# Kernel optimization log

Measured on AMD Instinct MI355X. Metric: run time of the kernel, lower is better.

## Reference

```python
import jax, jax.numpy as jnp
import numpy as np

# GlobalWorkspaceConfig constants (from init_kwargs)
DT_MS = 1.0
NMDA_TAU_MS = 100.0
IGNITE_THR = 0.58
WTA_INH = 0.85
K_SELECT = 2


def setup_inputs() -> dict:
    key = jax.random.key(0)
    k1, _ = jax.random.split(key)
    T, N = 8192, 4096
    # binary spikes with firing prob 0.7 so the EMA crosses ignite_thr=0.58
    spikes = (jax.random.uniform(k1, (T, N)) < 0.7).astype(jnp.float32)
    nmda0 = jnp.zeros((N,), jnp.float32)  # initial nmda_state buffer
    return {"spikes": spikes, "nmda0": nmda0}


def reference(spikes, nmda0):
    T, N = spikes.shape
    alpha = DT_MS / max(NMDA_TAU_MS, 1.0)  # 0.01

    # linear EMA recurrence: nmda_t = (1-alpha)*nmda_{t-1} + alpha*s_t
    def step(nmda, s_t):
        nmda = (1.0 - alpha) * nmda + alpha * s_t
        return nmda, nmda

    nmda_final, nmda_seq = jax.lax.scan(step, nmda0, spikes)  # nmda_seq: [T, N]

    # per-step ignition test: max over neurons vs threshold
    ignited = nmda_seq.max(axis=1) >= IGNITE_THR  # [T] bool

    # per-step top-k (k-WTA). wta_inh scaling kept for faithfulness.
    k = min(K_SELECT, N)
    scores = nmda_seq * WTA_INH
    _, idx = jax.lax.top_k(scores, k)  # [T, k]

    rows = jnp.arange(T)[:, None]
    ignite_mask = jnp.zeros((T, N), jnp.float32).at[rows, idx].set(1.0)
    ignite_mask = ignite_mask * ignited[:, None].astype(jnp.float32)

    # coverage = mean of the row mask = k/N when ignited, else 0
    coverage = jnp.where(ignited, jnp.float32(k) / jnp.float32(N), jnp.float32(0.0))

    return ignite_mask, coverage, nmda_final
```

## Files before the change

kernel.cpp:

```cpp
#include <hip/hip_runtime.h>
#include <cstdint>
#include <cstddef>

#define C_DECAY 0.99f
#define C_ALPHA 0.01f
#define C_THR   0.58f
#define C_WTA   0.85f

#define NPB   16
#define TILE  256

#define EMA_STEP(x) nmda = __fadd_rn(__fmul_rn(C_DECAY, nmda), __fmul_rn(C_ALPHA, (x)))

typedef const __attribute__((address_space(1))) void g_void;
typedef __attribute__((address_space(3))) void l_void;
typedef float f32x4 __attribute__((ext_vector_type(4)));

__device__ __forceinline__ void gload_lds16(const float* g, float* l) {
  __builtin_amdgcn_global_load_lds((g_void*)g, (l_void*)l, 16, 0, 0);
}

__global__ __launch_bounds__(128)
void gw_phase1(const float* __restrict__ spikes, const float* __restrict__ nmda0,
               float* __restrict__ bnd, float* __restrict__ nmf,
               int T, int N, int Ls) {
  __shared__ float sb[2][TILE * NPB];
  const int w    = threadIdx.x >> 6;
  const int lane = threadIdx.x & 63;
  const int nblk = gridDim.x;
  const int bs   = (nblk % 8 == 0) ? ((blockIdx.x & 7) * (nblk >> 3) + (blockIdx.x >> 3))
                                   : (int)blockIdx.x;
  const int n0   = bs * NPB;
  const int ntiles = T / TILE;
  const int Lm1  = (1 << Ls) - 1;
  const int grow = lane >> 2;
  const int gc   = (lane & 3) * 4;

  if (w == 1) {
#pragma unroll
    for (int j = 0; j < TILE / 16; ++j)
      gload_lds16(spikes + (size_t)(j * 16 + grow) * N + n0 + gc, &sb[0][j * 256]);
  }
  __syncthreads();

  const int nn = lane & (NPB - 1);
  float nmda = 0.0f;
  if (w == 0) nmda = nmda0[n0 + nn];

  for (int tile = 0; tile < ntiles; ++tile) {
    const int cur = tile & 1;
    if (w == 0) {
      const float* buf = sb[cur];
      const int t0 = tile * TILE;
      float tA[16], tB[16];
#pragma unroll
      for (int i = 0; i < 16; ++i) tA[i] = buf[i * NPB + nn];
#pragma unroll
      for (int jp = 0; jp < TILE / 32; ++jp) {
#pragma unroll
        for (int i = 0; i < 16; ++i) tB[i] = buf[((2 * jp + 1) * 16 + i) * NPB + nn];
        { const int tb = t0 + 2 * jp * 16;
          if ((tb & Lm1) == 0 && lane < NPB) bnd[(size_t)(tb >> Ls) * N + n0 + lane] = nmda; }
#pragma unroll
        for (int i = 0; i < 16; ++i) EMA_STEP(tA[i]);
        if (jp < TILE / 32 - 1) {
#pragma unroll
          for (int i = 0; i < 16; ++i) tA[i] = buf[((2 * jp + 2) * 16 + i) * NPB + nn];
        }
        { const int tb = t0 + (2 * jp + 1) * 16;
          if ((tb & Lm1) == 0 && lane < NPB) bnd[(size_t)(tb >> Ls) * N + n0 + lane] = nmda; }
#pragma unroll
        for (int i = 0; i < 16; ++i) EMA_STEP(tB[i]);
      }
    } else if (tile + 1 < ntiles) {
      const int t0 = (tile + 1) * TILE;
#pragma unroll
      for (int j = 0; j < TILE / 16; ++j)
        gload_lds16(spikes + (size_t)(t0 + j * 16 + grow) * N + n0 + gc, &sb[cur ^ 1][j * 256]);
    }
    __syncthreads();
  }
  if (w == 0 && lane < NPB) nmf[n0 + lane] = nmda;
}

__device__ __forceinline__ void merge2(float& a1, int& i1, float& a2, int& i2,
                                       float b1, int j1, float b2, int j2) {
  const bool afirst = (a1 > b1) || (a1 == b1 && i1 < j1);
  const float w1 = afirst ? a1 : b1; const int wi1 = afirst ? i1 : j1;
  const float l1 = afirst ? b1 : a1; const int li1 = afirst ? j1 : i1;
  const float cc = afirst ? a2 : b2; const int ci  = afirst ? i2 : j2;
  const bool sfirst = (cc > l1) || (cc == l1 && ci < li1);
  a1 = w1; i1 = wi1;
  a2 = sfirst ? cc : l1; i2 = sfirst ? ci : li1;
}

#define LOCAL_TOP2(c, idx)                                         \
  if ((c) > a1) { a2 = a1; i2 = i1; a1 = (c); i1 = (idx); }        \
  else if ((c) > a2) { a2 = (c); i2 = (idx); }

#define EMA_ROW(sA, sB)                                                        \
  nmA.x = __fadd_rn(__fmul_rn(C_DECAY, nmA.x), __fmul_rn(C_ALPHA, (sA).x));    \
  nmA.y = __fadd_rn(__fmul_rn(C_DECAY, nmA.y), __fmul_rn(C_ALPHA, (sA).y));    \
  nmA.z = __fadd_rn(__fmul_rn(C_DECAY, nmA.z), __fmul_rn(C_ALPHA, (sA).z));    \
  nmA.w = __fadd_rn(__fmul_rn(C_DECAY, nmA.w), __fmul_rn(C_ALPHA, (sA).w));    \
  nmB.x = __fadd_rn(__fmul_rn(C_DECAY, nmB.x), __fmul_rn(C_ALPHA, (sB).x));    \
  nmB.y = __fadd_rn(__fmul_rn(C_DECAY, nmB.y), __fmul_rn(C_ALPHA, (sB).y));    \
  nmB.z = __fadd_rn(__fmul_rn(C_DECAY, nmB.z), __fmul_rn(C_ALPHA, (sB).z));    \
  nmB.w = __fadd_rn(__fmul_rn(C_DECAY, nmB.w), __fmul_rn(C_ALPHA, (sB).w));

__global__ __launch_bounds__(512)
void gw_phase2s(const float* __restrict__ spikes, const float* __restrict__ bnd,
                float* __restrict__ mask, float* __restrict__ cov,
                int T, int N, float covval) {
  const int tid  = threadIdx.x;
  const int lane = tid & 63;
  const int wv   = tid >> 6;
  const int N4   = N >> 2;
  const int half = N4 >> 1;
  const float4* sp4 = (const float4*)spikes;
  f32x4* mk4 = (f32x4*)mask;

  __shared__ float ws1[8][64]; __shared__ int wi1s[8][64];
  __shared__ float ws2[8][64]; __shared__ int wi2s[8][64];
  __shared__ float wmx[8][64];
  __shared__ int gj1[8], gj2[8];

  const int chunk = blockIdx.x >> 1;
  const int h     = blockIdx.x & 1;
  float4 nmA = ((const float4*)bnd)[(size_t)chunk * N4 + tid];
  float4 nmB = ((const float4*)bnd)[(size_t)chunk * N4 + tid + half];
  const int baseA = tid * 4;
  const int baseB = baseA + (N >> 1);
  const int tc    = chunk * 16;

  if (h) {
    float4 pA[4], pB[4];
#pragma unroll
    for (int r = 0; r < 4; ++r) {
      pA[r] = sp4[(size_t)(tc + r) * N4 + tid];
      pB[r] = sp4[(size_t)(tc + r) * N4 + tid + half];
    }
#pragma unroll
    for (int r = 0; r < 8; ++r) {
      const float4 s  = pA[r & 3];
      const float4 s2 = pB[r & 3];
      if (r < 4) {
        pA[r & 3] = sp4[(size_t)(tc + r + 4) * N4 + tid];
        pB[r & 3] = sp4[(size_t)(tc + r + 4) * N4 + tid + half];
      }
      EMA_ROW(s, s2);
    }
  }
  const int tg = tc + h * 8;

  const int cslot = wv * 8 + (lane >> 3);
  float4 pA[4], pB[4];
#pragma unroll
  for (int r = 0; r < 4; ++r) {
    pA[r] = sp4[(size_t)(tg + r) * N4 + tid];
    pB[r] = sp4[(size_t)(tg + r) * N4 + tid + half];
  }
#pragma unroll
  for (int r = 0; r < 8; ++r) {
    const float4 s  = pA[r & 3];
    const float4 s2 = pB[r & 3];
    if (r < 4) {
      pA[r & 3] = sp4[(size_t)(tg + r + 4) * N4 + tid];
      pB[r & 3] = sp4[(size_t)(tg + r + 4) * N4 + tid + half];
    }

    EMA_ROW(s, s2);

    const float cA0 = __fmul_rn(nmA.x, C_WTA), cA1 = __fmul_rn(nmA.y, C_WTA);
    const float cA2 = __fmul_rn(nmA.z, C_WTA), cA3 = __fmul_rn(nmA.w, C_WTA);
    const float cB0 = __fmul_rn(nmB.x, C_WTA), cB1 = __fmul_rn(nmB.y, C_WTA);
    const float cB2 = __fmul_rn(nmB.z, C_WTA), cB3 = __fmul_rn(nmB.w, C_WTA);
    float mx = fmaxf(fmaxf(fmaxf(nmA.x, nmA.y), fmaxf(nmA.z, nmA.w)),
                     fmaxf(fmaxf(nmB.x, nmB.y), fmaxf(nmB.z, nmB.w)));

    float a1 = cA0; int i1 = baseA;
    float a2 = -__builtin_inff(); int i2 = 0x7fffffff;
    LOCAL_TOP2(cA1, baseA + 1); LOCAL_TOP2(cA2, baseA + 2); LOCAL_TOP2(cA3, baseA + 3);
    LOCAL_TOP2(cB0, baseB);     LOCAL_TOP2(cB1, baseB + 1);
    LOCAL_TOP2(cB2, baseB + 2); LOCAL_TOP2(cB3, baseB + 3);

#pragma unroll
    for (int m = 1; m < 8; m <<= 1) {
      const float b1 = __shfl_xor(a1, m, 64); const int j1 = __shfl_xor(i1, m, 64);
      const float b2 = __shfl_xor(a2, m, 64); const int j2 = __shfl_xor(i2, m, 64);
      mx = fmaxf(mx, __shfl_xor(mx, m, 64));
      merge2(a1, i1, a2, i2, b1, j1, b2, j2);
    }
    if ((lane & 7) == 0) {
      ws1[r][cslot] = a1; wi1s[r][cslot] = i1;
      ws2[r][cslot] = a2; wi2s[r][cslot] = i2;
      wmx[r][cslot] = mx;
    }
  }
  __syncthreads();

  {
    const int row = wv;
    float a1 = ws1[row][lane]; int i1 = wi1s[row][lane];
    float a2 = ws2[row][lane]; int i2 = wi2s[row][lane];
    float gm = wmx[row][lane];
#pragma unroll
    for (int m = 1; m < 64; m <<= 1) {
      const float b1 = __shfl_xor(a1, m, 64); const int j1 = __shfl_xor(i1, m, 64);
      const float b2 = __shfl_xor(a2, m, 64); const int j2 = __shfl_xor(i2, m, 64);
      gm = fmaxf(gm, __shfl_xor(gm, m, 64));
      merge2(a1, i1, a2, i2, b1, j1, b2, j2);
    }
    if (lane == 0) {
      const int ig = (gm >= C_THR) ? 1 : 0;
      gj1[row] = ig ? i1 : -1;
      gj2[row] = ig ? i2 : -1;
      cov[tg + row] = ig ? covval : 0.0f;
    }
  }
  __syncthreads();

#pragma unroll
  for (int r = 0; r < 8; ++r) {
    const int j1 = gj1[r], j2 = gj2[r];
    f32x4 v, u;
    v.x = (j1 == baseA     || j2 == baseA)     ? 1.0f : 0.0f;
    v.y = (j1 == baseA + 1 || j2 == baseA + 1) ? 1.0f : 0.0f;
    v.z = (j1 == baseA + 2 || j2 == baseA + 2) ? 1.0f : 0.0f;
    v.w = (j1 == baseA + 3 || j2 == baseA + 3) ? 1.0f : 0.0f;
    u.x = (j1 == baseB     || j2 == baseB)     ? 1.0f : 0.0f;
    u.y = (j1 == baseB + 1 || j2 == baseB + 1) ? 1.0f : 0.0f;
    u.z = (j1 == baseB + 2 || j2 == baseB + 2) ? 1.0f : 0.0f;
    u.w = (j1 == baseB + 3 || j2 == baseB + 3) ? 1.0f : 0.0f;
    __builtin_nontemporal_store(v, &mk4[(size_t)(tg + r) * N4 + tid]);
    __builtin_nontemporal_store(u, &mk4[(size_t)(tg + r) * N4 + tid + half]);
  }
}

template<int GR>
__global__ __launch_bounds__(512)
void gw_phase2(const float* __restrict__ spikes, const float* __restrict__ bnd,
               float* __restrict__ mask, float* __restrict__ cov,
               int T, int N, int L, float covval) {
  const int tid  = threadIdx.x;
  const int lane = tid & 63;
  const int wv   = tid >> 6;
  const int N4   = N >> 2;
  const int half = N4 >> 1;
  const float4* sp4 = (const float4*)spikes;
  f32x4* mk4 = (f32x4*)mask;

  __shared__ float ws1[GR][64]; __shared__ int wi1s[GR][64];
  __shared__ float ws2[GR][64]; __shared__ int wi2s[GR][64];
  __shared__ float wmx[GR][64];
  __shared__ int gj1[GR], gj2[GR];

  const int chunk = blockIdx.x;
  float4 nmA = ((const float4*)bnd)[(size_t)chunk * N4 + tid];
  float4 nmB = ((const float4*)bnd)[(size_t)chunk * N4 + tid + half];
  const int baseA = tid * 4;
  const int baseB = baseA + (N >> 1);
  const int t00   = chunk * L;
  const int cslot = wv * 8 + (lane >> 3);

  for (int g = 0; g < L; g += GR) {
    const int tg = t00 + g;
    float4 pA[4], pB[4];
#pragma unroll
    for (int r = 0; r < 4; ++r) {
      pA[r] = sp4[(size_t)(tg + r) * N4 + tid];
      pB[r] = sp4[(size_t)(tg + r) * N4 + tid + half];
    }
#pragma unroll
    for (int r = 0; r < GR; ++r) {
      const float4 s  = pA[r & 3];
      const float4 s2 = pB[r & 3];
      if (r < GR - 4) {
        pA[r & 3] = sp4[(size_t)(tg + r + 4) * N4 + tid];
        pB[r & 3] = sp4[(size_t)(tg + r + 4) * N4 + tid + half];
      }
      EMA_ROW(s, s2);
      const float cA0 = __fmul_rn(nmA.x, C_WTA), cA1 = __fmul_rn(nmA.y, C_WTA);
      const float cA2 = __fmul_rn(nmA.z, C_WTA), cA3 = __fmul_rn(nmA.w, C_WTA);
      const float cB0 = __fmul_rn(nmB.x, C_WTA), cB1 = __fmul_rn(nmB.y, C_WTA);
      const float cB2 = __fmul_rn(nmB.z, C_WTA), cB3 = __fmul_rn(nmB.w, C_WTA);
      float mx = fmaxf(fmaxf(fmaxf(nmA.x, nmA.y), fmaxf(nmA.z, nmA.w)),
                       fmaxf(fmaxf(nmB.x, nmB.y), fmaxf(nmB.z, nmB.w)));
      float a1 = cA0; int i1 = baseA;
      float a2 = -__builtin_inff(); int i2 = 0x7fffffff;
      LOCAL_TOP2(cA1, baseA + 1); LOCAL_TOP2(cA2, baseA + 2); LOCAL_TOP2(cA3, baseA + 3);
      LOCAL_TOP2(cB0, baseB);     LOCAL_TOP2(cB1, baseB + 1);
      LOCAL_TOP2(cB2, baseB + 2); LOCAL_TOP2(cB3, baseB + 3);
#pragma unroll
      for (int m = 1; m < 8; m <<= 1) {
        const float b1 = __shfl_xor(a1, m, 64); const int j1 = __shfl_xor(i1, m, 64);
        const float b2 = __shfl_xor(a2, m, 64); const int j2 = __shfl_xor(i2, m, 64);
        mx = fmaxf(mx, __shfl_xor(mx, m, 64));
        merge2(a1, i1, a2, i2, b1, j1, b2, j2);
      }
      if ((lane & 7) == 0) {
        ws1[r][cslot] = a1; wi1s[r][cslot] = i1;
        ws2[r][cslot] = a2; wi2s[r][cslot] = i2;
        wmx[r][cslot] = mx;
      }
    }
    __syncthreads();
#pragma unroll
    for (int rr = 0; rr < GR / 8; ++rr) {
      const int row = wv * (GR / 8) + rr;
      float a1 = ws1[row][lane]; int i1 = wi1s[row][lane];
      float a2 = ws2[row][lane]; int i2 = wi2s[row][lane];
      float gm = wmx[row][lane];
#pragma unroll
      for (int m = 1; m < 64; m <<= 1) {
        const float b1 = __shfl_xor(a1, m, 64); const int j1 = __shfl_xor(i1, m, 64);
        const float b2 = __shfl_xor(a2, m, 64); const int j2 = __shfl_xor(i2, m, 64);
        gm = fmaxf(gm, __shfl_xor(gm, m, 64));
        merge2(a1, i1, a2, i2, b1, j1, b2, j2);
      }
      if (lane == 0) {
        const int ig = (gm >= C_THR) ? 1 : 0;
        gj1[row] = ig ? i1 : -1;
        gj2[row] = ig ? i2 : -1;
        cov[tg + row] = ig ? covval : 0.0f;
      }
    }
    __syncthreads();
#pragma unroll
    for (int r = 0; r < GR; ++r) {
      const int j1 = gj1[r], j2 = gj2[r];
      f32x4 v, u;
      v.x = (j1 == baseA     || j2 == baseA)     ? 1.0f : 0.0f;
      v.y = (j1 == baseA + 1 || j2 == baseA + 1) ? 1.0f : 0.0f;
      v.z = (j1 == baseA + 2 || j2 == baseA + 2) ? 1.0f : 0.0f;
      v.w = (j1 == baseA + 3 || j2 == baseA + 3) ? 1.0f : 0.0f;
      u.x = (j1 == baseB     || j2 == baseB)     ? 1.0f : 0.0f;
      u.y = (j1 == baseB + 1 || j2 == baseB + 1) ? 1.0f : 0.0f;
      u.z = (j1 == baseB + 2 || j2 == baseB + 2) ? 1.0f : 0.0f;
      u.w = (j1 == baseB + 3 || j2 == baseB + 3) ? 1.0f : 0.0f;
      __builtin_nontemporal_store(v, &mk4[(size_t)(tg + r) * N4 + tid]);
      __builtin_nontemporal_store(u, &mk4[(size_t)(tg + r) * N4 + tid + half]);
    }
    if (g + GR < L) __syncthreads();
  }
}

extern "C" void kernel_launch(void* const* d_in, const int* in_sizes, int n_in,
                              void* d_out, int out_size, void* d_ws, size_t ws_size,
                              hipStream_t stream) {
  const float* spikes = (const float*)d_in[0];
  const float* nmda0  = (const float*)d_in[1];
  const int N = in_sizes[1];
  const int T = in_sizes[0] / N;

  float* out  = (float*)d_out;
  float* mask = out;
  float* cov  = out + (size_t)T * N;
  float* nmf  = cov + T;

  int Ls = 4;
  while (((size_t)(T >> Ls)) * (size_t)N * sizeof(float) > ws_size && Ls < 13) ++Ls;
  const int L = 1 << Ls;
  const int C = T >> Ls;
  float* bnd = (float*)d_ws;
  const float covval = 2.0f / (float)N;

  gw_phase1<<<N / NPB, 128, 0, stream>>>(spikes, nmda0, bnd, nmf, T, N, Ls);
  if (L == 16)
    gw_phase2s<<<2 * C, 512, 0, stream>>>(spikes, bnd, mask, cov, T, N, covval);
  else if (L % 8 == 0)
    gw_phase2<8><<<C, 512, 0, stream>>>(spikes, bnd, mask, cov, T, N, L, covval);
  else
    gw_phase2<16><<<C, 512, 0, stream>>>(spikes, bnd, mask, cov, T, N, L, covval);
}
```

Baseline: 122.3 us.

## Store mid-chunk EMA checkpoints in phase1 so phase2 skips re-scanning half chunks

Phase 1 now also saves the EMA state at the midpoint of every 16-row chunk (every 8 rows) into a second workspace buffer. Phase 2 can then start each 8-row block straight from a stored checkpoint, so the odd half-chunk blocks no longer re-read 8 extra spike rows to catch up. This cuts phase-2 spike reads and serial EMA work. In exchange phase 1 writes twice as many checkpoints, and the workspace must hold twice as much; otherwise the code falls back to the older path.

```diff
diff --git a/kernel.cpp b/kernel.cpp
--- a/kernel.cpp
+++ b/kernel.cpp
@@ -22,8 +22,8 @@
 
 __global__ __launch_bounds__(128)
 void gw_phase1(const float* __restrict__ spikes, const float* __restrict__ nmda0,
-               float* __restrict__ bnd, float* __restrict__ nmf,
-               int T, int N, int Ls) {
+               float* __restrict__ bnd, float* __restrict__ bndh,
+               float* __restrict__ nmf, int T, int N, int Ls) {
   __shared__ float sb[2][TILE * NPB];
   const int w    = threadIdx.x >> 6;
   const int lane = threadIdx.x & 63;
@@ -52,7 +52,7 @@
     if (w == 0) {
       const float* buf = sb[cur];
       const int t0 = tile * TILE;
-      float tA[16], tB[16];
+      float tA[16], tB[16], sv[16];
 #pragma unroll
       for (int i = 0; i < 16; ++i) tA[i] = buf[i * NPB + nn];
 #pragma unroll
@@ -62,7 +62,10 @@
         { const int tb = t0 + 2 * jp * 16;
           if ((tb & Lm1) == 0 && lane < NPB) bnd[(size_t)(tb >> Ls) * N + n0 + lane] = nmda; }
 #pragma unroll
-        for (int i = 0; i < 16; ++i) EMA_STEP(tA[i]);
+        for (int i = 0; i < 8; ++i) EMA_STEP(tA[i]);
+        sv[2 * jp] = nmda;
+#pragma unroll
+        for (int i = 8; i < 16; ++i) EMA_STEP(tA[i]);
         if (jp < TILE / 32 - 1) {
 #pragma unroll
           for (int i = 0; i < 16; ++i) tA[i] = buf[((2 * jp + 2) * 16 + i) * NPB + nn];
@@ -70,7 +73,15 @@
         { const int tb = t0 + (2 * jp + 1) * 16;
           if ((tb & Lm1) == 0 && lane < NPB) bnd[(size_t)(tb >> Ls) * N + n0 + lane] = nmda; }
 #pragma unroll
-        for (int i = 0; i < 16; ++i) EMA_STEP(tB[i]);
+        for (int i = 0; i < 8; ++i) EMA_STEP(tB[i]);
+        sv[2 * jp + 1] = nmda;
+#pragma unroll
+        for (int i = 8; i < 16; ++i) EMA_STEP(tB[i]);
+      }
+      if (bndh != nullptr && lane < NPB) {
+#pragma unroll
+        for (int g2 = 0; g2 < 16; ++g2)
+          bndh[(size_t)(t0 / 16 + g2) * N + n0 + lane] = sv[g2];
       }
     } else if (tile + 1 < ntiles) {
       const int t0 = (tile + 1) * TILE;
@@ -109,7 +120,8 @@
   nmB.w = __fadd_rn(__fmul_rn(C_DECAY, nmB.w), __fmul_rn(C_ALPHA, (sB).w));
 
 __global__ __launch_bounds__(512)
-void gw_phase2s(const float* __restrict__ spikes, const float* __restrict__ bnd,
+void gw_phase2p(const float* __restrict__ spikes, const float* __restrict__ bnd,
+                const float* __restrict__ bndh,
                 float* __restrict__ mask, float* __restrict__ cov,
                 int T, int N, float covval) {
   const int tid  = threadIdx.x;
@@ -125,35 +137,16 @@
   __shared__ float wmx[8][64];
   __shared__ int gj1[8], gj2[8];
 
-  const int chunk = blockIdx.x >> 1;
-  const int h     = blockIdx.x & 1;
-  float4 nmA = ((const float4*)bnd)[(size_t)chunk * N4 + tid];
-  float4 nmB = ((const float4*)bnd)[(size_t)chunk * N4 + tid + half];
+  const int chunk = blockIdx.x;
+  const int k     = chunk >> 1;
+  const float4* src = (chunk & 1) ? (const float4*)bndh : (const float4*)bnd;
+  float4 nmA = src[(size_t)k * N4 + tid];
+  float4 nmB = src[(size_t)k * N4 + tid + half];
   const int baseA = tid * 4;
   const int baseB = baseA + (N >> 1);
-  const int tc    = chunk * 16;
-
-  if (h) {
-    float4 pA[4], pB[4];
-#pragma unroll
-    for (int r = 0; r < 4; ++r) {
-      pA[r] = sp4[(size_t)(tc + r) * N4 + tid];
-      pB[r] = sp4[(size_t)(tc + r) * N4 + tid + half];
-    }
-#pragma unroll
-    for (int r = 0; r < 8; ++r) {
-      const float4 s  = pA[r & 3];
-      const float4 s2 = pB[r & 3];
-      if (r < 4) {
-        pA[r & 3] = sp4[(size_t)(tc + r + 4) * N4 + tid];
-        pB[r & 3] = sp4[(size_t)(tc + r + 4) * N4 + tid + half];
-      }
-      EMA_ROW(s, s2);
-    }
-  }
-  const int tg = tc + h * 8;
-
+  const int tg    = chunk * 8;
   const int cslot = wv * 8 + (lane >> 3);
+
   float4 pA[4], pB[4];
 #pragma unroll
   for (int r = 0; r < 4; ++r) {
@@ -357,19 +350,27 @@
   float* mask = out;
   float* cov  = out + (size_t)T * N;
   float* nmf  = cov + T;
-
-  int Ls = 4;
-  while (((size_t)(T >> Ls)) * (size_t)N * sizeof(float) > ws_size && Ls < 13) ++Ls;
-  const int L = 1 << Ls;
-  const int C = T >> Ls;
-  float* bnd = (float*)d_ws;
   const float covval = 2.0f / (float)N;
 
-  gw_phase1<<<N / NPB, 128, 0, stream>>>(spikes, nmda0, bnd, nmf, T, N, Ls);
-  if (L == 16)
-    gw_phase2s<<<2 * C, 512, 0, stream>>>(spikes, bnd, mask, cov, T, N, covval);
-  else if (L % 8 == 0)
-    gw_phase2<8><<<C, 512, 0, stream>>>(spikes, bnd, mask, cov, T, N, L, covval);
-  else
-    gw_phase2<16><<<C, 512, 0, stream>>>(spikes, bnd, mask, cov, T, N, L, covval);
-}
+  const int C16 = T >> 4;
+  const size_t need2 = 2 * (size_t)C16 * N * sizeof(float);
+  const bool split = (T % (2 * TILE) == 0) && (need2 <= ws_size);
+
+  if (split) {
+    float* bnd  = (float*)d_ws;
+    float* bndh = bnd + (size_t)C16 * N;
+    gw_phase1<<<N / NPB, 128, 0, stream>>>(spikes, nmda0, bnd, bndh, nmf, T, N, 4);
+    gw_phase2p<<<T / 8, 512, 0, stream>>>(spikes, bnd, bndh, mask, cov, T, N, covval);
+  } else {
+    int Ls = 4;
+    while (((size_t)(T >> Ls)) * (size_t)N * sizeof(float) > ws_size && Ls < 13) ++Ls;
+    const int L = 1 << Ls;
+    const int C = T >> Ls;
+    float* bnd = (float*)d_ws;
+    gw_phase1<<<N / NPB, 128, 0, stream>>>(spikes, nmda0, bnd, nullptr, nmf, T, N, Ls);
+    if (L % 8 == 0 && L % 16 != 0)
+      gw_phase2<8><<<C, 512, 0, stream>>>(spikes, bnd, mask, cov, T, N, L, covval);
+    else
+      gw_phase2<16><<<C, 512, 0, stream>>>(spikes, bnd, mask, cov, T, N, L, covval);
+  }
+}
```

New measurement: 116.0 us. -5.2%, faster.
